# Performance work log

Hardware: AMD Instinct MI355X
Metric: run time of the kernel (lower is better)

Reference implementation:

```python
import jax, jax.numpy as jnp
import numpy as np
from jax import lax

NUM_CLASSES = 9
N_BOXES = 6
LEVELS = [(32, 256), (16, 128), (8, 64), (4, 32), (2, 16), (1, 8)]
BATCH = 8


def _conv(x, w, b):
    # x: [N,C,H,W], w: [O,I,3,3] -> same-padded stride-1 conv (padding=1)
    y = lax.conv_general_dilated(x, w, window_strides=(1, 1), padding='SAME',
                                 dimension_numbers=('NCHW', 'OIHW', 'NCHW'))
    return y + b[None, :, None, None]


def _head(x, ws, bs, w_out, b_out):
    for i in range(4):
        x = jax.nn.relu(_conv(x, ws[i], bs[i]))
    return _conv(x, w_out, b_out)


def setup_inputs() -> dict:
    key = jax.random.key(0)
    ks = jax.random.split(key, 12)
    inp = {}
    for i, (h, w) in enumerate(LEVELS):
        inp[f'feat{i}'] = jax.random.normal(ks[i], (BATCH, 256, h, w), dtype=jnp.float32)
    std = 0.01  # matches _init_improved_weights: normal(0, 0.01), bias=0
    inp['reg_w'] = jax.random.normal(ks[6], (4, 256, 256, 3, 3), dtype=jnp.float32) * std
    inp['reg_b'] = jnp.zeros((4, 256), dtype=jnp.float32)
    inp['reg_w_out'] = jax.random.normal(ks[7], (N_BOXES * 4, 256, 3, 3), dtype=jnp.float32) * std
    inp['reg_b_out'] = jnp.zeros((N_BOXES * 4,), dtype=jnp.float32)
    inp['cls_w'] = jax.random.normal(ks[8], (4, 256, 256, 3, 3), dtype=jnp.float32) * std
    inp['cls_b'] = jnp.zeros((4, 256), dtype=jnp.float32)
    inp['cls_w_out'] = jax.random.normal(ks[9], (N_BOXES * NUM_CLASSES, 256, 3, 3), dtype=jnp.float32) * std
    inp['cls_b_out'] = jnp.zeros((N_BOXES * NUM_CLASSES,), dtype=jnp.float32)
    return inp


def reference(feat0, feat1, feat2, feat3, feat4, feat5,
              reg_w, reg_b, reg_w_out, reg_b_out,
              cls_w, cls_b, cls_w_out, cls_b_out):
    features = [feat0, feat1, feat2, feat3, feat4, feat5]
    locations, confidences = [], []
    for x in features:
        n = x.shape[0]
        bbox_delta = _head(x, reg_w, reg_b, reg_w_out, reg_b_out).reshape(n, 4, -1)
        bbox_conf = _head(x, cls_w, cls_b, cls_w_out, cls_b_out).reshape(n, NUM_CLASSES, -1)
        locations.append(bbox_delta)
        confidences.append(bbox_conf)
    bbox_delta = jnp.concatenate(locations, axis=2)   # [N, 4, total_anchors]
    confs = jnp.concatenate(confidences, axis=2)      # [N, num_classes, total_anchors]
    return (bbox_delta, confs)
```

## Files before the change

### kernel.cpp

```cpp
#include <hip/hip_runtime.h>
#include <hip/hip_bf16.h>


typedef float  f32x4 __attribute__((ext_vector_type(4)));
typedef int    i32x4 __attribute__((ext_vector_type(4)));
typedef int    i32x2 __attribute__((ext_vector_type(2)));
typedef __bf16 bfrag __attribute__((ext_vector_type(8)));
typedef __bf16 bf4   __attribute__((ext_vector_type(4)));

struct LevelD {
  int H, W, logW, logHW, P, HW, act_off, aoff, blk_start, pos_start;
};
struct Desc  { LevelD lv[6]; };
struct FPtrs { const float* f[6]; };

#define ACT_ELEMS  24735744
#define WREG_OFF   0
#define WCLS_OFF   2359296
#define WREGO_OFF  4718592
#define WCLSO_OFF  4773888
#define ACT0_OFF   4898304
#define ACT1_OFF   29634048
#define ACT2_OFF   54369792
#define WS_ELEMS   54369792ull
#define TOTAL_ANCH 65520
#define CLS_BASE   2096640
#define NPAD_JOBS  9264

__device__ __forceinline__ void glds16(const __bf16* g, __bf16* l) {
  __builtin_amdgcn_global_load_lds(
      (const __attribute__((address_space(1))) void*)g,
      (__attribute__((address_space(3))) void*)l, 16, 0, 0);
}

__device__ __forceinline__ int xcd_swz(int b, int nwg) {
  int xcd = b & 7;
  int q = nwg >> 3, r = nwg & 7;
  int base = (xcd < r) ? xcd * (q + 1) : r * (q + 1) + (xcd - r) * q;
  return base + (b >> 3);
}

__global__ __launch_bounds__(256) void padzero_k(__bf16* __restrict__ act, int nbuf)
{
  static const int kHh[6]   = {32, 16, 8, 4, 2, 1};
  static const int kWw[6]   = {256, 128, 64, 32, 16, 8};
  static const int kOff[6]  = {0, 17965056, 22757376, 24109056, 24526848, 24674304};
  static const int kPer[6]  = {580, 292, 148, 76, 40, 22};
  static const int kCum[7]  = {0, 4640, 6976, 8160, 8768, 9088, 9264};
  int job  = blockIdx.x * 4 + (threadIdx.x >> 6);
  int lane = threadIdx.x & 63;
  int nb = job / NPAD_JOBS;
  if (nb >= nbuf) return;
  int e8 = job - nb * NPAD_JOBS;
  int li = 0;
  #pragma unroll
  for (int i = 1; i < 6; ++i) li = (e8 >= kCum[i]) ? i : li;
  int r = e8 - kCum[li];
  int per = kPer[li];
  int n = r / per;
  int e = r - n * per;
  int H = kHh[li], W = kWw[li], Wp = W + 2;
  int y, x;
  if (e < 2 * Wp) {
    y = (e < Wp) ? 0 : (H + 1);
    x = (e < Wp) ? e : (e - Wp);
  } else {
    int e2 = e - 2 * Wp;
    x = (e2 < H) ? 0 : (W + 1);
    y = 1 + ((e2 < H) ? e2 : (e2 - H));
  }
  size_t base = (size_t)nb * ACT_ELEMS + kOff[li]
              + ((size_t)((n * (H + 2) + y) * Wp + x) << 8) + (lane << 2);
  i32x2 z = {0, 0};
  *(i32x2*)(act + base) = z;
}

__global__ __launch_bounds__(256) void prep_k(const float* __restrict__ w,
                                              __bf16* __restrict__ o, int total)
{
  for (int i = blockIdx.x * 256 + threadIdx.x; i < total; i += gridDim.x * 256) {
    int co = i / 2304;
    int r  = i - co * 2304;
    int t  = r >> 8;
    int ci = r & 255;
    o[i] = (__bf16)w[((co << 8) + ci) * 9 + t];
  }
}

__global__ __launch_bounds__(256) void convert_k(FPtrs fp, __bf16* __restrict__ act, Desc d)
{
  __shared__ __bf16 T[16 * 264];
  int b  = blockIdx.x;
  int p0 = b << 4;
  int li = 0;
  #pragma unroll
  for (int i = 1; i < 6; ++i) li = (p0 >= d.lv[i].pos_start) ? i : li;
  LevelD L = d.lv[li];
  int lp  = b * 16 - L.pos_start;
  int tid = threadIdx.x;
  int pl = tid & 15;
  int p  = lp + pl;
  int n  = p >> L.logHW;
  int y  = (p >> L.logW) & (L.H - 1);
  int x  = p & (L.W - 1);
  const float* src = fp.f[li];
  size_t base = (size_t)n * ((size_t)L.HW << 8) + (size_t)y * L.W + x;
  int c0 = tid >> 4;
  #pragma unroll
  for (int it = 0; it < 16; ++it) {
    int c = c0 + (it << 4);
    T[pl * 264 + c] = (__bf16)src[base + (size_t)c * L.HW];
  }
  __syncthreads();
  int p2 = tid >> 4;
  int cc = (tid & 15) << 4;
  int pg = lp + p2;
  int n2 = pg >> L.logHW;
  int y2 = (pg >> L.logW) & (L.H - 1);
  int x2 = pg & (L.W - 1);
  __bf16* dst = act + L.act_off +
      ((size_t)((n2 * (L.H + 2) + y2 + 1) * (L.W + 2) + x2 + 1) << 8) + cc;
  i32x4 v0 = *(const i32x4*)&T[p2 * 264 + cc];
  i32x4 v1 = *(const i32x4*)&T[p2 * 264 + cc + 8];
  *(i32x4*)dst       = v0;
  *(i32x4*)(dst + 8) = v1;
}

__global__ __launch_bounds__(512, 4)
void conv_mid_k(const __bf16* __restrict__ inb, __bf16* __restrict__ outb,
                const __bf16* __restrict__ wT, const float* __restrict__ bias,
                Desc d)
{
  __shared__ __bf16 Asm[3][8192];
  __shared__ __bf16 Bsm[3][3072];
  int b  = xcd_swz(blockIdx.x, 912);
  int li = 0;
  #pragma unroll
  for (int i = 1; i < 6; ++i) li = (b >= d.lv[i].blk_start) ? i : li;
  LevelD L = d.lv[li];
  int p0 = (b - L.blk_start) * 96;
  int tid  = threadIdx.x;
  int lane = tid & 63;
  int wv   = tid >> 6;
  int wm = wv >> 1, wn = wv & 1;
  int fr = lane & 15, fg = lane >> 4;
  int Wp = L.W + 2;

  const __bf16* gA[2];
  int ldsA[2];
  #pragma unroll
  for (int r = 0; r < 2; ++r) {
    int row = (r << 7) + (wv << 4) + (lane >> 2);
    int sw  = (lane & 3) ^ ((row >> 1) & 3);
    gA[r] = wT + row * 2304 + (sw << 3);
    ldsA[r] = ((r << 7) + (wv << 4)) << 5;
  }
  bool bact = lane < 48;
  const __bf16* gB;
  int ldsB;
  {
    int row = wv * 12 + (lane >> 2);
    int sw  = (lane & 3) ^ ((row >> 1) & 3);
    int p  = p0 + row;
    int pc = (p < L.P) ? p : 0;
    int n  = pc >> L.logHW;
    int y  = (pc >> L.logW) & (L.H - 1);
    int x  = pc & (L.W - 1);
    gB = inb + L.act_off + (((n * (L.H + 2) + y) * Wp + x) << 8) + (sw << 3);
    ldsB = (wv * 12) << 5;
  }

  int offA[4], offB[3];
  #pragma unroll
  for (int mf = 0; mf < 4; ++mf) {
    int row = (wm << 6) + (mf << 4) + fr;
    offA[mf] = (row << 5) + ((fg ^ ((fr >> 1) & 3)) << 3);
  }
  #pragma unroll
  for (int nf = 0; nf < 3; ++nf) {
    int row = wn * 48 + (nf << 4) + fr;
    offB[nf] = (row << 5) + ((fg ^ ((fr >> 1) & 3)) << 3);
  }

  auto stage = [&](int kt, int buf) {
    int ko = ((kt >> 3) << 8) + ((kt & 7) << 5);
    glds16(gA[0] + ko, &Asm[buf][ldsA[0]]);
    glds16(gA[1] + ko, &Asm[buf][ldsA[1]]);
    int t  = kt >> 3;
    int ky = (t >= 6) ? 2 : (t >= 3 ? 1 : 0);
    int kx = t - ky * 3;
    int kb = ((ky * Wp + kx) << 8) + ((kt & 7) << 5);
    if (bact) glds16(gB + kb, &Bsm[buf][ldsB]);
  };

  f32x4 acc[4][3] = {};

  stage(0, 0);
  stage(1, 1);

  int cur = 0;
  #pragma unroll 1
  for (int kt = 0; kt < 72; ++kt) {
    int sbuf = cur + 2; if (sbuf >= 3) sbuf -= 3;
    if (kt == 71) { asm volatile("s_waitcnt vmcnt(0)" ::: "memory"); }
    else          { asm volatile("s_waitcnt vmcnt(3)" ::: "memory"); }
    __builtin_amdgcn_s_barrier();
    asm volatile("" ::: "memory");

    bfrag bf3[3], a0, a1, a2, a3;
    #pragma unroll
    for (int nf = 0; nf < 3; ++nf) bf3[nf] = *(const bfrag*)&Bsm[cur][offB[nf]];
    a0 = *(const bfrag*)&Asm[cur][offA[0]];
    a1 = *(const bfrag*)&Asm[cur][offA[1]];
    a2 = *(const bfrag*)&Asm[cur][offA[2]];
    a3 = *(const bfrag*)&Asm[cur][offA[3]];
    if (kt < 70) stage(kt + 2, sbuf);
    __builtin_amdgcn_s_setprio(1);
    #pragma unroll
    for (int nf = 0; nf < 3; ++nf) {
      acc[0][nf] = __builtin_amdgcn_mfma_f32_16x16x32_bf16(a0, bf3[nf], acc[0][nf], 0, 0, 0);
      acc[1][nf] = __builtin_amdgcn_mfma_f32_16x16x32_bf16(a1, bf3[nf], acc[1][nf], 0, 0, 0);
      acc[2][nf] = __builtin_amdgcn_mfma_f32_16x16x32_bf16(a2, bf3[nf], acc[2][nf], 0, 0, 0);
      acc[3][nf] = __builtin_amdgcn_mfma_f32_16x16x32_bf16(a3, bf3[nf], acc[3][nf], 0, 0, 0);
    }
    __builtin_amdgcn_s_setprio(0);

    ++cur; if (cur == 3) cur = 0;
  }

  #pragma unroll
  for (int nf = 0; nf < 3; ++nf) {
    int pp = p0 + wn * 48 + (nf << 4) + fr;
    if (pp >= L.P) continue;
    int n2 = pp >> L.logHW;
    int y2 = (pp >> L.logW) & (L.H - 1);
    int x2 = pp & (L.W - 1);
    __bf16* ob = outb + L.act_off + (((n2 * (L.H + 2) + y2 + 1) * Wp + x2 + 1) << 8);
    #pragma unroll
    for (int mf = 0; mf < 4; ++mf) {
      int cob = (wm << 6) + (mf << 4) + (fg << 2);
      f32x4 bb = *(const f32x4*)(bias + cob);
      f32x4 v  = acc[mf][nf];
      bf4 ov;
      #pragma unroll
      for (int j = 0; j < 4; ++j) ov[j] = (__bf16)fmaxf(v[j] + bb[j], 0.0f);
      *(bf4*)(ob + cob) = ov;
    }
  }
}

__global__ __launch_bounds__(256, 3)
void conv_out_k(const __bf16* __restrict__ inb, const __bf16* __restrict__ wT,
                const float* __restrict__ biasO, float* __restrict__ dout,
                Desc d, int Cout, int isCls)
{
  __shared__ __bf16 Asm[2][64 * 32];
  __shared__ __bf16 Bsm[2][128 * 32];
  int b  = xcd_swz(blockIdx.x, 683);
  int li = 0;
  #pragma unroll
  for (int i = 1; i < 6; ++i) li = (b >= d.lv[i].blk_start) ? i : li;
  LevelD L = d.lv[li];
  int p0 = (b - L.blk_start) << 7;
  int tid  = threadIdx.x;
  int lane = tid & 63;
  int wv   = tid >> 6;
  int fr = lane & 15, fg = lane >> 4;
  int Wp = L.W + 2;
  int nmf = (Cout + 15) >> 4;

  int rsub = lane >> 2;
  int slot = lane & 3;
  int sw   = slot ^ ((rsub >> 1) & 3);

  const __bf16* gA0;
  {
    int row = (wv << 4) + rsub;
    int co  = (row < Cout) ? row : 0;
    gA0 = wT + co * 2304 + (sw << 3);
  }
  const __bf16* gB[2];
  #pragma unroll
  for (int j = 0; j < 2; ++j) {
    int row = (j << 6) + (wv << 4) + rsub;
    int p  = p0 + row;
    int pc = (p < L.P) ? p : 0;
    int n = pc >> L.logHW, y = (pc >> L.logW) & (L.H - 1), x = pc & (L.W - 1);
    gB[j] = inb + L.act_off + (((n * (L.H + 2) + y) * Wp + x) << 8) + (sw << 3);
  }
  int dW = (wv << 4) << 5;

  int csw = ((fg ^ ((fr >> 1) & 3)) << 3);
  int offA[4], offB[2];
  #pragma unroll
  for (int mf = 0; mf < 4; ++mf)
    offA[mf] = (((mf << 4) + fr) << 5) + csw;
  #pragma unroll
  for (int nf = 0; nf < 2; ++nf)
    offB[nf] = (((wv << 5) + (nf << 4) + fr) << 5) + csw;

  auto stage = [&](int k, int bb) {
    int t  = k >> 3;
    int ky = (t >= 6) ? 2 : (t >= 3 ? 1 : 0);
    int kx = t - ky * 3;
    int ka = (t << 8) + ((k & 7) << 5);
    int kb = ((ky * Wp + kx) << 8) + ((k & 7) << 5);
    glds16(gA0 + ka, &Asm[bb][dW]);
    glds16(gB[0] + kb, &Bsm[bb][dW]);
    glds16(gB[1] + kb, &Bsm[bb][2048 + dW]);
  };

  f32x4 acc[4][2] = {};

  stage(0, 0);
  #pragma unroll 1
  for (int k = 0; k < 72; ++k) {
    int cur = k & 1;
    __syncthreads();
    if (k < 71) stage(k + 1, cur ^ 1);
    bfrag af[4], bfv[2];
    #pragma unroll
    for (int mf = 0; mf < 4; ++mf)
      if (mf < nmf) af[mf] = *(const bfrag*)&Asm[cur][offA[mf]];
    #pragma unroll
    for (int nf = 0; nf < 2; ++nf)
      bfv[nf] = *(const bfrag*)&Bsm[cur][offB[nf]];
    #pragma unroll
    for (int mf = 0; mf < 4; ++mf)
      if (mf < nmf)
        #pragma unroll
        for (int nf = 0; nf < 2; ++nf)
          acc[mf][nf] = __builtin_amdgcn_mfma_f32_16x16x32_bf16(
              af[mf], bfv[nf], acc[mf][nf], 0, 0, 0);
  }

  #pragma unroll
  for (int nf = 0; nf < 2; ++nf) {
    int pp = p0 + (wv << 5) + (nf << 4) + fr;
    if (pp >= L.P) continue;
    int n2 = pp >> L.logHW;
    int y2 = (pp >> L.logW) & (L.H - 1);
    int x2 = pp & (L.W - 1);
    int sp_off = L.aoff + y2 * L.W + x2;
    #pragma unroll
    for (int mf = 0; mf < 4; ++mf) {
      if (mf < nmf) {
        #pragma unroll
        for (int j = 0; j < 4; ++j) {
          int co = (mf << 4) + (fg << 2) + j;
          if (co < Cout) {
            float val = acc[mf][nf][j] + biasO[co];
            int g   = co / 6;
            int box = co - g * 6;
            size_t idx;
            if (isCls) idx = (size_t)CLS_BASE + ((size_t)n2 * 9 + g) * TOTAL_ANCH
                             + sp_off + box * L.HW;
            else       idx = ((size_t)n2 * 4 + g) * TOTAL_ANCH + sp_off + box * L.HW;
            dout[idx] = val;
          }
        }
      }
    }
  }
}

extern "C" void kernel_launch(void* const* d_in, const int* in_sizes, int n_in,
                              void* d_out, int out_size, void* d_ws, size_t ws_size,
                              hipStream_t stream) {
  if (ws_size < WS_ELEMS * 2) return;

  static const int kH[6]      = {32, 16, 8, 4, 2, 1};
  static const int kW[6]      = {256, 128, 64, 32, 16, 8};
  static const int kLogW[6]   = {8, 7, 6, 5, 4, 3};
  static const int kLogHW[6]  = {13, 11, 9, 7, 5, 3};
  static const int kActOff[6] = {0, 17965056, 22757376, 24109056, 24526848, 24674304};
  static const int kAoff[6]   = {0, 49152, 61440, 64512, 65280, 65472};
  static const int kBlkMid[6] = {0, 683, 854, 897, 908, 911};
  static const int kBlkOut[6] = {0, 512, 640, 672, 680, 682};
  static const int kPosSt[6]  = {0, 65536, 81920, 86016, 87040, 87296};

  FPtrs fp;
  for (int i = 0; i < 6; ++i) fp.f[i] = (const float*)d_in[i];
  const float* reg_w  = (const float*)d_in[6];
  const float* reg_b  = (const float*)d_in[7];
  const float* reg_wo = (const float*)d_in[8];
  const float* reg_bo = (const float*)d_in[9];
  const float* cls_w  = (const float*)d_in[10];
  const float* cls_b  = (const float*)d_in[11];
  const float* cls_wo = (const float*)d_in[12];
  const float* cls_bo = (const float*)d_in[13];
  __bf16* ws = (__bf16*)d_ws;

  Desc dmid, dout_d;
  for (int i = 0; i < 6; ++i) {
    LevelD L;
    L.H = kH[i]; L.W = kW[i]; L.logW = kLogW[i]; L.logHW = kLogHW[i];
    L.HW = kH[i] * kW[i]; L.P = 8 * L.HW;
    L.act_off = kActOff[i]; L.aoff = kAoff[i];
    L.pos_start = kPosSt[i];
    L.blk_start = kBlkMid[i];
    dmid.lv[i] = L;
    L.blk_start = kBlkOut[i];
    dout_d.lv[i] = L;
  }

  bool use3 = ws_size >= (size_t)(ACT0_OFF + 3ull * ACT_ELEMS) * 2ull;
  int nbuf = use3 ? 3 : 2;

  padzero_k<<<(NPAD_JOBS * nbuf + 3) / 4, 256, 0, stream>>>(ws + ACT0_OFF, nbuf);

  prep_k<<<256, 256, 0, stream>>>(reg_w,  ws + WREG_OFF,  1024 * 2304);
  prep_k<<<256, 256, 0, stream>>>(cls_w,  ws + WCLS_OFF,  1024 * 2304);
  prep_k<<<64,  256, 0, stream>>>(reg_wo, ws + WREGO_OFF, 24 * 2304);
  prep_k<<<64,  256, 0, stream>>>(cls_wo, ws + WCLSO_OFF, 54 * 2304);

  if (use3) {
    convert_k<<<5460, 256, 0, stream>>>(fp, ws + ACT2_OFF, dmid);
    for (int head = 0; head < 2; ++head) {
      const __bf16* wT = ws + (head ? WCLS_OFF : WREG_OFF);
      const float*  bb = head ? cls_b : reg_b;
      conv_mid_k<<<912, 512, 0, stream>>>(ws + ACT2_OFF, ws + ACT0_OFF, wT + 0 * 589824, bb + 0,   dmid);
      conv_mid_k<<<912, 512, 0, stream>>>(ws + ACT0_OFF, ws + ACT1_OFF, wT + 1 * 589824, bb + 256, dmid);
      conv_mid_k<<<912, 512, 0, stream>>>(ws + ACT1_OFF, ws + ACT0_OFF, wT + 2 * 589824, bb + 512, dmid);
      conv_mid_k<<<912, 512, 0, stream>>>(ws + ACT0_OFF, ws + ACT1_OFF, wT + 3 * 589824, bb + 768, dmid);
      conv_out_k<<<683, 256, 0, stream>>>(ws + ACT1_OFF,
          ws + (head ? WCLSO_OFF : WREGO_OFF), head ? cls_bo : reg_bo,
          (float*)d_out, dout_d, head ? 54 : 24, head);
    }
  } else {
    for (int head = 0; head < 2; ++head) {
      convert_k<<<5460, 256, 0, stream>>>(fp, ws + ACT0_OFF, dmid);
      const __bf16* wT = ws + (head ? WCLS_OFF : WREG_OFF);
      const float*  bb = head ? cls_b : reg_b;
      conv_mid_k<<<912, 512, 0, stream>>>(ws + ACT0_OFF, ws + ACT1_OFF, wT + 0 * 589824, bb + 0,   dmid);
      conv_mid_k<<<912, 512, 0, stream>>>(ws + ACT1_OFF, ws + ACT0_OFF, wT + 1 * 589824, bb + 256, dmid);
      conv_mid_k<<<912, 512, 0, stream>>>(ws + ACT0_OFF, ws + ACT1_OFF, wT + 2 * 589824, bb + 512, dmid);
      conv_mid_k<<<912, 512, 0, stream>>>(ws + ACT1_OFF, ws + ACT0_OFF, wT + 3 * 589824, bb + 768, dmid);
      conv_out_k<<<683, 256, 0, stream>>>(ws + ACT0_OFF,
          ws + (head ? WCLSO_OFF : WREGO_OFF), head ? cls_bo : reg_bo,
          (float*)d_out, dout_d, head ? 54 : 24, head);
    }
  }
}
```

Before: 1.195 ms.

## Load conv weight fragments directly from global into registers, bypassing LDS

The weight (A) operand of the mid-layer conv GEMM is no longer staged through a triple-buffered LDS array. Each wave now loads its own MFMA A fragments straight from global memory into registers, one k-step ahead, while the activation (B) tile keeps its LDS pipeline. This frees 48 KB of shared memory per block and removes the A LDS reads, which could raise occupancy. In exchange each wave issues redundant, poorly coalesced global loads (rows 2304 elements apart), and the vmcnt waits are hand-tuned and fragile.

```diff
diff --git a/kernel.cpp b/kernel.cpp
--- a/kernel.cpp
+++ b/kernel.cpp
@@ -131,7 +131,6 @@
                 const __bf16* __restrict__ wT, const float* __restrict__ bias,
                 Desc d)
 {
-  __shared__ __bf16 Asm[3][8192];
   __shared__ __bf16 Bsm[3][3072];
   int b  = xcd_swz(blockIdx.x, 912);
   int li = 0;
@@ -146,15 +145,6 @@
   int fr = lane & 15, fg = lane >> 4;
   int Wp = L.W + 2;
 
-  const __bf16* gA[2];
-  int ldsA[2];
-  #pragma unroll
-  for (int r = 0; r < 2; ++r) {
-    int row = (r << 7) + (wv << 4) + (lane >> 2);
-    int sw  = (lane & 3) ^ ((row >> 1) & 3);
-    gA[r] = wT + row * 2304 + (sw << 3);
-    ldsA[r] = ((r << 7) + (wv << 4)) << 5;
-  }
   bool bact = lane < 48;
   const __bf16* gB;
   int ldsB;
@@ -170,22 +160,19 @@
     ldsB = (wv * 12) << 5;
   }
 
-  int offA[4], offB[3];
-  #pragma unroll
-  for (int mf = 0; mf < 4; ++mf) {
-    int row = (wm << 6) + (mf << 4) + fr;
-    offA[mf] = (row << 5) + ((fg ^ ((fr >> 1) & 3)) << 3);
-  }
+  const __bf16* aG0 = wT + ((wm << 6) + 0  + fr) * 2304 + (fg << 3);
+  const __bf16* aG1 = wT + ((wm << 6) + 16 + fr) * 2304 + (fg << 3);
+  const __bf16* aG2 = wT + ((wm << 6) + 32 + fr) * 2304 + (fg << 3);
+  const __bf16* aG3 = wT + ((wm << 6) + 48 + fr) * 2304 + (fg << 3);
+
+  int offB[3];
   #pragma unroll
   for (int nf = 0; nf < 3; ++nf) {
     int row = wn * 48 + (nf << 4) + fr;
     offB[nf] = (row << 5) + ((fg ^ ((fr >> 1) & 3)) << 3);
   }
 
-  auto stage = [&](int kt, int buf) {
-    int ko = ((kt >> 3) << 8) + ((kt & 7) << 5);
-    glds16(gA[0] + ko, &Asm[buf][ldsA[0]]);
-    glds16(gA[1] + ko, &Asm[buf][ldsA[1]]);
+  auto stageB = [&](int kt, int buf) {
     int t  = kt >> 3;
     int ky = (t >= 6) ? 2 : (t >= 3 ? 1 : 0);
     int kx = t - ky * 3;
@@ -195,36 +182,50 @@
 
   f32x4 acc[4][3] = {};
 
-  stage(0, 0);
-  stage(1, 1);
+  stageB(0, 0);
+  stageB(1, 1);
+  asm volatile("" ::: "memory");
+  bfrag cA0 = *(const bfrag*)aG0;
+  bfrag cA1 = *(const bfrag*)aG1;
+  bfrag cA2 = *(const bfrag*)aG2;
+  bfrag cA3 = *(const bfrag*)aG3;
 
   int cur = 0;
   #pragma unroll 1
   for (int kt = 0; kt < 72; ++kt) {
     int sbuf = cur + 2; if (sbuf >= 3) sbuf -= 3;
-    if (kt == 71) { asm volatile("s_waitcnt vmcnt(0)" ::: "memory"); }
-    else          { asm volatile("s_waitcnt vmcnt(3)" ::: "memory"); }
+    if (kt == 71) { asm volatile("s_waitcnt vmcnt(4)" ::: "memory"); }
+    else          { asm volatile("s_waitcnt vmcnt(5)" ::: "memory"); }
     __builtin_amdgcn_s_barrier();
     asm volatile("" ::: "memory");
 
-    bfrag bf3[3], a0, a1, a2, a3;
+    bfrag bf3[3];
     #pragma unroll
     for (int nf = 0; nf < 3; ++nf) bf3[nf] = *(const bfrag*)&Bsm[cur][offB[nf]];
-    a0 = *(const bfrag*)&Asm[cur][offA[0]];
-    a1 = *(const bfrag*)&Asm[cur][offA[1]];
-    a2 = *(const bfrag*)&Asm[cur][offA[2]];
-    a3 = *(const bfrag*)&Asm[cur][offA[3]];
-    if (kt < 70) stage(kt + 2, sbuf);
+    if (kt < 70) stageB(kt + 2, sbuf);
+
+    bfrag pA0, pA1, pA2, pA3;
+    if (kt < 71) {
+      int ko = (kt + 1) << 5;
+      pA0 = *(const bfrag*)(aG0 + ko);
+      pA1 = *(const bfrag*)(aG1 + ko);
+      pA2 = *(const bfrag*)(aG2 + ko);
+      pA3 = *(const bfrag*)(aG3 + ko);
+    } else {
+      pA0 = cA0; pA1 = cA1; pA2 = cA2; pA3 = cA3;
+    }
+
     __builtin_amdgcn_s_setprio(1);
     #pragma unroll
     for (int nf = 0; nf < 3; ++nf) {
-      acc[0][nf] = __builtin_amdgcn_mfma_f32_16x16x32_bf16(a0, bf3[nf], acc[0][nf], 0, 0, 0);
-      acc[1][nf] = __builtin_amdgcn_mfma_f32_16x16x32_bf16(a1, bf3[nf], acc[1][nf], 0, 0, 0);
-      acc[2][nf] = __builtin_amdgcn_mfma_f32_16x16x32_bf16(a2, bf3[nf], acc[2][nf], 0, 0, 0);
-      acc[3][nf] = __builtin_amdgcn_mfma_f32_16x16x32_bf16(a3, bf3[nf], acc[3][nf], 0, 0, 0);
+      acc[0][nf] = __builtin_amdgcn_mfma_f32_16x16x32_bf16(cA0, bf3[nf], acc[0][nf], 0, 0, 0);
+      acc[1][nf] = __builtin_amdgcn_mfma_f32_16x16x32_bf16(cA1, bf3[nf], acc[1][nf], 0, 0, 0);
+      acc[2][nf] = __builtin_amdgcn_mfma_f32_16x16x32_bf16(cA2, bf3[nf], acc[2][nf], 0, 0, 0);
+      acc[3][nf] = __builtin_amdgcn_mfma_f32_16x16x32_bf16(cA3, bf3[nf], acc[3][nf], 0, 0, 0);
     }
     __builtin_amdgcn_s_setprio(0);
 
+    cA0 = pA0; cA1 = pA1; cA2 = pA2; cA3 = pA3;
     ++cur; if (cur == 3) cur = 0;
   }
 
```

After: 2.597 ms. 2.17x slower.
